# Kernel optimization log

Measured on AMD Instinct MI355X. Metric: run time of the kernel, lower is better.

## Reference

```python
import jax, jax.numpy as jnp
import numpy as np

B, H, L, D = 2, 16, 2048, 64
P = 2            # pos_dim
F = D // 2       # rotation pairs
MIN_FREQ, MAX_FREQ = 0.5, 40.0


def setup_inputs() -> dict:
    key = jax.random.key(0)
    kq, kk, kv, kf = jax.random.split(key, 4)
    query = jax.random.normal(kq, (B, H, L, D), dtype=jnp.float32)
    key_t = jax.random.normal(kk, (B, H, L, D), dtype=jnp.float32)
    value = jax.random.normal(kv, (B, H, L, D), dtype=jnp.float32)
    # default positions per _ensure_pos: arange(L) broadcast to [B, L, P]
    pos = jnp.broadcast_to(jnp.arange(L, dtype=jnp.float32)[None, :, None], (B, L, P))
    # normalize to [0,1) grid-like coords as typical for 2D RoPE in diffusion
    pos = pos / jnp.float32(L)
    # golden-gate-style freqs: log-spaced magnitudes x random unit directions, per head
    mags = jnp.exp(jnp.linspace(jnp.log(MIN_FREQ), jnp.log(MAX_FREQ), F, dtype=jnp.float32))  # [F]
    dirs = jax.random.normal(kf, (H, F, P), dtype=jnp.float32)
    dirs = dirs / jnp.linalg.norm(dirs, axis=-1, keepdims=True)
    freqs_hfp = dirs * (2.0 * jnp.pi * mags)[None, :, None]  # [H, F, P]
    return {"query": query, "key": key_t, "value": value, "pos": pos, "freqs_hfp": freqs_hfp}


def _apply_rope(x, theta):
    # x: [B,H,L,D], theta: [B,H,L,F]; rotate-half convention (first/second halves paired)
    x1, x2 = x[..., :F], x[..., F:]
    c, s = jnp.cos(theta), jnp.sin(theta)
    return jnp.concatenate([x1 * c - x2 * s, x2 * c + x1 * s], axis=-1)


def reference(query, key, value, pos, freqs_hfp):
    # RoPE angles: contract positions against per-head freq directions
    theta = jnp.einsum("blp,hfp->bhlf", pos, freqs_hfp)  # [B,H,L,F]
    q_rot = _apply_rope(query, theta)
    k_rot = _apply_rope(key, theta)
    # FlexAttention with noop score_mod == standard scaled softmax attention
    scale = 1.0 / jnp.sqrt(jnp.float32(D))
    scores = jnp.einsum("bhld,bhmd->bhlm", q_rot, k_rot) * scale  # [B,H,L,L]
    probs = jax.nn.softmax(scores, axis=-1)
    out = jnp.einsum("bhlm,bhmd->bhld", probs, value)
    return out
```

## Files before the change

### kernel.cpp

```cpp
#include <hip/hip_runtime.h>
#include <math.h>

constexpr int B_ = 2, H_ = 16, L_ = 2048, D_ = 64, F_ = 32;
constexpr int BH_ = B_ * H_;
constexpr float SCALE_LOG2E = 0.125f * 1.44269504088896340736f;
constexpr float INV_2PI = 0.15915494309189535f;
constexpr float MSTATIC = 8.0f;

using half8   = __attribute__((ext_vector_type(8))) _Float16;
using floatx16 = __attribute__((ext_vector_type(16))) float;
using uint2v  = __attribute__((ext_vector_type(2))) unsigned int;
typedef unsigned int u32;

__device__ inline float fexp2(float x) { return __builtin_amdgcn_exp2f(x); }
__device__ inline floatx16 splat16(float v) {
  floatx16 r;
  #pragma unroll
  for (int i = 0; i < 16; ++i) r[i] = v;
  return r;
}

__global__ __launch_bounds__(256) void rope_v_prepass(
    const float* __restrict__ q, const float* __restrict__ k,
    const float* __restrict__ v, const float* __restrict__ pos,
    const float* __restrict__ freqs,
    _Float16* __restrict__ qr, _Float16* __restrict__ kr,
    _Float16* __restrict__ vt) {
  __shared__ _Float16 vls[64][66];

  const int tid  = threadIdx.x;
  const int r0   = blockIdx.x * 64;
  const int lrow = tid >> 2;
  const int j    = tid & 3;
  const int row  = r0 + lrow;
  const int l    = row % L_;
  const int h    = (row / L_) % H_;
  const int b    = row / (H_ * L_);

  const float p0 = pos[(b * L_ + l) * 2 + 0];
  const float p1 = pos[(b * L_ + l) * 2 + 1];

  float c[8], s[8];
  #pragma unroll
  for (int i = 0; i < 8; ++i) {
    const int f = j * 8 + i;
    const float th = p0 * freqs[(h * F_ + f) * 2 + 0] +
                     p1 * freqs[(h * F_ + f) * 2 + 1];
    float t = th * INV_2PI;
    t -= rintf(t);
    c[i] = __builtin_amdgcn_cosf(t);
    s[i] = __builtin_amdgcn_sinf(t);
  }

  const float* qrow = q + (size_t)row * D_;
  const float* krow = k + (size_t)row * D_;

  {
    float x1[8], x2[8];
    *(float4*)(x1)     = *(const float4*)(qrow + j * 8);
    *(float4*)(x1 + 4) = *(const float4*)(qrow + j * 8 + 4);
    *(float4*)(x2)     = *(const float4*)(qrow + j * 8 + 32);
    *(float4*)(x2 + 4) = *(const float4*)(qrow + j * 8 + 36);
    half8 o1, o2;
    #pragma unroll
    for (int i = 0; i < 8; ++i) {
      o1[i] = (_Float16)((x1[i] * c[i] - x2[i] * s[i]) * SCALE_LOG2E);
      o2[i] = (_Float16)((x2[i] * c[i] + x1[i] * s[i]) * SCALE_LOG2E);
    }
    *(half8*)(qr + (size_t)row * D_ + j * 8)      = o1;
    *(half8*)(qr + (size_t)row * D_ + 32 + j * 8) = o2;
  }
  {
    float x1[8], x2[8];
    *(float4*)(x1)     = *(const float4*)(krow + j * 8);
    *(float4*)(x1 + 4) = *(const float4*)(krow + j * 8 + 4);
    *(float4*)(x2)     = *(const float4*)(krow + j * 8 + 32);
    *(float4*)(x2 + 4) = *(const float4*)(krow + j * 8 + 36);
    half8 o1, o2;
    #pragma unroll
    for (int i = 0; i < 8; ++i) {
      o1[i] = (_Float16)(x1[i] * c[i] - x2[i] * s[i]);
      o2[i] = (_Float16)(x2[i] * c[i] + x1[i] * s[i]);
    }
    *(half8*)(kr + (size_t)row * D_ + j * 8)      = o1;
    *(half8*)(kr + (size_t)row * D_ + 32 + j * 8) = o2;
  }

  const float* vrow = v + (size_t)row * D_;
  #pragma unroll
  for (int i4 = 0; i4 < 4; ++i4) {
    float4 vv = *(const float4*)(vrow + j * 16 + i4 * 4);
    vls[lrow][j * 16 + i4 * 4 + 0] = (_Float16)vv.x;
    vls[lrow][j * 16 + i4 * 4 + 1] = (_Float16)vv.y;
    vls[lrow][j * 16 + i4 * 4 + 2] = (_Float16)vv.z;
    vls[lrow][j * 16 + i4 * 4 + 3] = (_Float16)vv.w;
  }
  __syncthreads();
  const int d  = tid >> 2;
  const int jj = tid & 3;
  const int bh = b * H_ + h;
  half8 w0, w1;
  #pragma unroll
  for (int i = 0; i < 8; ++i) {
    w0[i] = vls[jj * 16 + i][d];
    w1[i] = vls[jj * 16 + 8 + i][d];
  }
  const size_t vtoff = ((size_t)bh * D_ + d) * L_ + (size_t)(r0 % L_) + jj * 16;
  *(half8*)(vt + vtoff)     = w0;
  *(half8*)(vt + vtoff + 8) = w1;
}

__global__ __launch_bounds__(256, 2) void flash_attn(
    const _Float16* __restrict__ qr, const _Float16* __restrict__ kr,
    const _Float16* __restrict__ vt, float* __restrict__ out) {
  __shared__ _Float16 Kl[2][128 * 64];
  __shared__ _Float16 Vl[2][64 * 128];

  const int bid  = blockIdx.x;
  const int wg   = (bid & 7) * 64 + (bid >> 3);
  const int head = wg >> 4;
  const int qb   = wg & 15;

  const int tid  = threadIdx.x;
  const int wid  = tid >> 6;
  const int lane = tid & 63;
  const int ql   = lane & 31;
  const int hi   = lane >> 5;

  const _Float16* qbase =
      qr + ((size_t)head * L_ + (size_t)(qb * 128 + wid * 32 + ql)) * D_;
  half8 qf[4];
  #pragma unroll
  for (int c = 0; c < 4; ++c) qf[c] = *(const half8*)(qbase + c * 16 + hi * 8);

  floatx16 o0 = {}, o1 = {};
  float lsumL = 0.f;

  const _Float16* kb = kr + (size_t)head * L_ * D_;
  const _Float16* vb = vt + (size_t)head * D_ * L_;

  int koff[4], voff[8];
  #pragma unroll
  for (int c = 0; c < 4; ++c)
    koff[c] = (ql * 128 + c * 32 + hi * 16) ^ ((ql & 7) << 4);
  #pragma unroll
  for (int kc = 0; kc < 8; ++kc)
    voff[kc] = (ql * 256 + kc * 32 + hi * 16) ^ ((ql & 15) << 4);

  constexpr int NT = L_ / 256;

  for (int t = 0; t < NT; ++t) {
    __syncthreads();
    #pragma unroll
    for (int h = 0; h < 2; ++h) {
      #pragma unroll
      for (int ci = 0; ci < 4; ++ci) {
        const int c = tid + ci * 256;
        const int krw = c >> 3, kcc = c & 7, kcd = kcc ^ (krw & 7);
        const uint4 dk = *(const uint4*)(
            kb + (size_t)(t * 256 + h * 128 + krw) * D_ + kcd * 8);
        *(uint4*)((char*)&Kl[h][0] + krw * 128 + kcc * 16) = dk;
        const int vrw = c >> 4, vcc = c & 15, vcd = vcc ^ (vrw & 15);
        const uint4 dv = *(const uint4*)(
            vb + (size_t)vrw * L_ + t * 256 + h * 128 + vcd * 8);
        *(uint4*)((char*)&Vl[h][0] + vrw * 256 + vcc * 16) = dv;
      }
    }
    __syncthreads();

    #pragma unroll
    for (int h = 0; h < 2; ++h) {
      const char* kbuf = (const char*)&Kl[h][0];
      const char* vbuf = (const char*)&Vl[h][0];

      floatx16 s0 = splat16(-MSTATIC), s1 = splat16(-MSTATIC);
      floatx16 s2 = splat16(-MSTATIC), s3 = splat16(-MSTATIC);
      #pragma unroll
      for (int c = 0; c < 4; ++c) {
        const half8 k0 = *(const half8*)(kbuf + koff[c]);
        const half8 k1 = *(const half8*)(kbuf + koff[c] + 4096);
        const half8 k2 = *(const half8*)(kbuf + koff[c] + 8192);
        const half8 k3 = *(const half8*)(kbuf + koff[c] + 12288);
        s0 = __builtin_amdgcn_mfma_f32_32x32x16_f16(k0, qf[c], s0, 0, 0, 0);
        s1 = __builtin_amdgcn_mfma_f32_32x32x16_f16(k1, qf[c], s1, 0, 0, 0);
        s2 = __builtin_amdgcn_mfma_f32_32x32x16_f16(k2, qf[c], s2, 0, 0, 0);
        s3 = __builtin_amdgcn_mfma_f32_32x32x16_f16(k3, qf[c], s3, 0, 0, 0);
      }

      float sm[16];
      #pragma unroll
      for (int r = 0; r < 16; ++r) {
        s0[r] = fexp2(s0[r]);
        s1[r] = fexp2(s1[r]);
        s2[r] = fexp2(s2[r]);
        s3[r] = fexp2(s3[r]);
        sm[r] = (s0[r] + s1[r]) + (s2[r] + s3[r]);
      }
      #pragma unroll
      for (int st = 8; st > 0; st >>= 1)
        #pragma unroll
        for (int r = 0; r < 8; ++r)
          if (r < st) sm[r] += sm[r + st];
      lsumL += sm[0];

      u32 w[4][8];
      #pragma unroll
      for (int u = 0; u < 8; ++u) {
        w[0][u] = __builtin_bit_cast(u32,
                    __builtin_amdgcn_cvt_pkrtz(s0[2 * u], s0[2 * u + 1]));
        w[1][u] = __builtin_bit_cast(u32,
                    __builtin_amdgcn_cvt_pkrtz(s1[2 * u], s1[2 * u + 1]));
        w[2][u] = __builtin_bit_cast(u32,
                    __builtin_amdgcn_cvt_pkrtz(s2[2 * u], s2[2 * u + 1]));
        w[3][u] = __builtin_bit_cast(u32,
                    __builtin_amdgcn_cvt_pkrtz(s3[2 * u], s3[2 * u + 1]));
      }

      #pragma unroll
      for (int tt = 0; tt < 4; ++tt) {
        #pragma unroll
        for (int kcl = 0; kcl < 2; ++kcl) {
          const uint2v ra = __builtin_amdgcn_permlane32_swap(
              w[tt][4 * kcl + 0], w[tt][4 * kcl + 2], false, false);
          const uint2v rb = __builtin_amdgcn_permlane32_swap(
              w[tt][4 * kcl + 1], w[tt][4 * kcl + 3], false, false);
          uint4 bfw; bfw.x = ra.x; bfw.y = rb.x; bfw.z = ra.y; bfw.w = rb.y;
          const half8 pf = __builtin_bit_cast(half8, bfw);
          const int kc = tt * 2 + kcl;
          const half8 v0 = *(const half8*)(vbuf + voff[kc]);
          const half8 v1 = *(const half8*)(vbuf + voff[kc] + 8192);
          o0 = __builtin_amdgcn_mfma_f32_32x32x16_f16(v0, pf, o0, 0, 0, 0);
          o1 = __builtin_amdgcn_mfma_f32_32x32x16_f16(v1, pf, o1, 0, 0, 0);
        }
      }
    }
  }

  const float lsum = lsumL + __shfl_xor(lsumL, 32);
  const float inv = 1.0f / lsum;
  float* ob = out + ((size_t)head * L_ + (size_t)(qb * 128 + wid * 32 + ql)) * D_;
  #pragma unroll
  for (int b = 0; b < 4; ++b) {
    float4 v0, v1;
    v0.x = o0[4 * b + 0] * inv; v0.y = o0[4 * b + 1] * inv;
    v0.z = o0[4 * b + 2] * inv; v0.w = o0[4 * b + 3] * inv;
    v1.x = o1[4 * b + 0] * inv; v1.y = o1[4 * b + 1] * inv;
    v1.z = o1[4 * b + 2] * inv; v1.w = o1[4 * b + 3] * inv;
    *(float4*)(ob + 8 * b + 4 * hi)      = v0;
    *(float4*)(ob + 32 + 8 * b + 4 * hi) = v1;
  }
}

extern "C" void kernel_launch(void* const* d_in, const int* in_sizes, int n_in,
                              void* d_out, int out_size, void* d_ws, size_t ws_size,
                              hipStream_t stream) {
  const float* q     = (const float*)d_in[0];
  const float* k     = (const float*)d_in[1];
  const float* v     = (const float*)d_in[2];
  const float* pos   = (const float*)d_in[3];
  const float* freqs = (const float*)d_in[4];
  float* out = (float*)d_out;

  _Float16* qr = (_Float16*)d_ws;
  _Float16* kr = qr + (size_t)BH_ * L_ * D_;
  _Float16* vt = kr + (size_t)BH_ * L_ * D_;

  const int rows = B_ * H_ * L_;
  rope_v_prepass<<<rows / 64, 256, 0, stream>>>(q, k, v, pos, freqs, qr, kr, vt);

  const int nwg = BH_ * (L_ / 128);
  flash_attn<<<nwg, 256, 0, stream>>>(qr, kr, vt, out);
}
```

Before: 61.75 us.

## Split KV sequence across two wave groups per block with LDS reduction

Doubles the block to 512 threads and splits the 2048 keys into two halves, each processed by a group of four waves with its own K/V LDS tiles. At the end the partial outputs and row sums from the second group are merged through shared memory before normalisation. This raises waves per block and per CU so more memory latency can be hidden, at the cost of a cross-group reduction, 64KB of LDS per block, and a launch bound of 4 waves per SIMD that may limit registers.

```diff
diff --git a/kernel.cpp b/kernel.cpp
--- a/kernel.cpp
+++ b/kernel.cpp
@@ -110,11 +110,10 @@
   *(half8*)(vt + vtoff + 8) = w1;
 }
 
-__global__ __launch_bounds__(256, 2) void flash_attn(
+__global__ __launch_bounds__(512, 4) void flash_attn(
     const _Float16* __restrict__ qr, const _Float16* __restrict__ kr,
     const _Float16* __restrict__ vt, float* __restrict__ out) {
-  __shared__ _Float16 Kl[2][128 * 64];
-  __shared__ _Float16 Vl[2][64 * 128];
+  __shared__ char smem[65536];
 
   const int bid  = blockIdx.x;
   const int wg   = (bid & 7) * 64 + (bid >> 3);
@@ -123,12 +122,18 @@
 
   const int tid  = threadIdx.x;
   const int wid  = tid >> 6;
+  const int g    = wid >> 2;
+  const int wq   = wid & 3;
   const int lane = tid & 63;
   const int ql   = lane & 31;
   const int hi   = lane >> 5;
+  const int gtid = tid & 255;
+
+  char* kbuf = smem + g * 16384;
+  char* vbuf = smem + 32768 + g * 16384;
 
   const _Float16* qbase =
-      qr + ((size_t)head * L_ + (size_t)(qb * 128 + wid * 32 + ql)) * D_;
+      qr + ((size_t)head * L_ + (size_t)(qb * 128 + wq * 32 + ql)) * D_;
   half8 qf[4];
   #pragma unroll
   for (int c = 0; c < 4; ++c) qf[c] = *(const half8*)(qbase + c * 16 + hi * 8);
@@ -136,8 +141,9 @@
   floatx16 o0 = {}, o1 = {};
   float lsumL = 0.f;
 
-  const _Float16* kb = kr + (size_t)head * L_ * D_;
+  const _Float16* kb = kr + (size_t)head * L_ * D_ + (size_t)(g * 1024) * D_;
   const _Float16* vb = vt + (size_t)head * D_ * L_;
+  const int vcol0 = g * 1024;
 
   int koff[4], voff[8];
   #pragma unroll
@@ -147,107 +153,118 @@
   for (int kc = 0; kc < 8; ++kc)
     voff[kc] = (ql * 256 + kc * 32 + hi * 16) ^ ((ql & 15) << 4);
 
-  constexpr int NT = L_ / 256;
+  constexpr int NT = 1024 / 128;
 
   for (int t = 0; t < NT; ++t) {
     __syncthreads();
     #pragma unroll
-    for (int h = 0; h < 2; ++h) {
+    for (int ci = 0; ci < 4; ++ci) {
+      const int c = gtid + ci * 256;
+      const int krw = c >> 3, kcc = c & 7, kcd = kcc ^ (krw & 7);
+      const uint4 dk =
+          *(const uint4*)(kb + (size_t)(t * 128 + krw) * D_ + kcd * 8);
+      *(uint4*)(kbuf + krw * 128 + kcc * 16) = dk;
+      const int vrw = c >> 4, vcc = c & 15, vcd = vcc ^ (vrw & 15);
+      const uint4 dv = *(const uint4*)(
+          vb + (size_t)vrw * L_ + vcol0 + t * 128 + vcd * 8);
+      *(uint4*)(vbuf + vrw * 256 + vcc * 16) = dv;
+    }
+    __syncthreads();
+
+    floatx16 s0 = splat16(-MSTATIC), s1 = splat16(-MSTATIC);
+    floatx16 s2 = splat16(-MSTATIC), s3 = splat16(-MSTATIC);
+    #pragma unroll
+    for (int c = 0; c < 4; ++c) {
+      const half8 k0 = *(const half8*)(kbuf + koff[c]);
+      const half8 k1 = *(const half8*)(kbuf + koff[c] + 4096);
+      const half8 k2 = *(const half8*)(kbuf + koff[c] + 8192);
+      const half8 k3 = *(const half8*)(kbuf + koff[c] + 12288);
+      s0 = __builtin_amdgcn_mfma_f32_32x32x16_f16(k0, qf[c], s0, 0, 0, 0);
+      s1 = __builtin_amdgcn_mfma_f32_32x32x16_f16(k1, qf[c], s1, 0, 0, 0);
+      s2 = __builtin_amdgcn_mfma_f32_32x32x16_f16(k2, qf[c], s2, 0, 0, 0);
+      s3 = __builtin_amdgcn_mfma_f32_32x32x16_f16(k3, qf[c], s3, 0, 0, 0);
+    }
+
+    float sm[16];
+    #pragma unroll
+    for (int r = 0; r < 16; ++r) {
+      s0[r] = fexp2(s0[r]);
+      s1[r] = fexp2(s1[r]);
+      s2[r] = fexp2(s2[r]);
+      s3[r] = fexp2(s3[r]);
+      sm[r] = (s0[r] + s1[r]) + (s2[r] + s3[r]);
+    }
+    #pragma unroll
+    for (int st = 8; st > 0; st >>= 1)
       #pragma unroll
-      for (int ci = 0; ci < 4; ++ci) {
-        const int c = tid + ci * 256;
-        const int krw = c >> 3, kcc = c & 7, kcd = kcc ^ (krw & 7);
-        const uint4 dk = *(const uint4*)(
-            kb + (size_t)(t * 256 + h * 128 + krw) * D_ + kcd * 8);
-        *(uint4*)((char*)&Kl[h][0] + krw * 128 + kcc * 16) = dk;
-        const int vrw = c >> 4, vcc = c & 15, vcd = vcc ^ (vrw & 15);
-        const uint4 dv = *(const uint4*)(
-            vb + (size_t)vrw * L_ + t * 256 + h * 128 + vcd * 8);
-        *(uint4*)((char*)&Vl[h][0] + vrw * 256 + vcc * 16) = dv;
+      for (int r = 0; r < 8; ++r)
+        if (r < st) sm[r] += sm[r + st];
+    lsumL += sm[0];
+
+    u32 w[4][8];
+    #pragma unroll
+    for (int u = 0; u < 8; ++u) {
+      w[0][u] = __builtin_bit_cast(u32,
+                  __builtin_amdgcn_cvt_pkrtz(s0[2 * u], s0[2 * u + 1]));
+      w[1][u] = __builtin_bit_cast(u32,
+                  __builtin_amdgcn_cvt_pkrtz(s1[2 * u], s1[2 * u + 1]));
+      w[2][u] = __builtin_bit_cast(u32,
+                  __builtin_amdgcn_cvt_pkrtz(s2[2 * u], s2[2 * u + 1]));
+      w[3][u] = __builtin_bit_cast(u32,
+                  __builtin_amdgcn_cvt_pkrtz(s3[2 * u], s3[2 * u + 1]));
+    }
+
+    #pragma unroll
+    for (int tt = 0; tt < 4; ++tt) {
+      #pragma unroll
+      for (int kcl = 0; kcl < 2; ++kcl) {
+        const uint2v ra = __builtin_amdgcn_permlane32_swap(
+            w[tt][4 * kcl + 0], w[tt][4 * kcl + 2], false, false);
+        const uint2v rb = __builtin_amdgcn_permlane32_swap(
+            w[tt][4 * kcl + 1], w[tt][4 * kcl + 3], false, false);
+        uint4 bfw; bfw.x = ra.x; bfw.y = rb.x; bfw.z = ra.y; bfw.w = rb.y;
+        const half8 pf = __builtin_bit_cast(half8, bfw);
+        const int kc = tt * 2 + kcl;
+        const half8 v0 = *(const half8*)(vbuf + voff[kc]);
+        const half8 v1 = *(const half8*)(vbuf + voff[kc] + 8192);
+        o0 = __builtin_amdgcn_mfma_f32_32x32x16_f16(v0, pf, o0, 0, 0, 0);
+        o1 = __builtin_amdgcn_mfma_f32_32x32x16_f16(v1, pf, o1, 0, 0, 0);
       }
     }
-    __syncthreads();
-
-    #pragma unroll
-    for (int h = 0; h < 2; ++h) {
-      const char* kbuf = (const char*)&Kl[h][0];
-      const char* vbuf = (const char*)&Vl[h][0];
-
-      floatx16 s0 = splat16(-MSTATIC), s1 = splat16(-MSTATIC);
-      floatx16 s2 = splat16(-MSTATIC), s3 = splat16(-MSTATIC);
-      #pragma unroll
-      for (int c = 0; c < 4; ++c) {
-        const half8 k0 = *(const half8*)(kbuf + koff[c]);
-        const half8 k1 = *(const half8*)(kbuf + koff[c] + 4096);
-        const half8 k2 = *(const half8*)(kbuf + koff[c] + 8192);
-        const half8 k3 = *(const half8*)(kbuf + koff[c] + 12288);
-        s0 = __builtin_amdgcn_mfma_f32_32x32x16_f16(k0, qf[c], s0, 0, 0, 0);
-        s1 = __builtin_amdgcn_mfma_f32_32x32x16_f16(k1, qf[c], s1, 0, 0, 0);
-        s2 = __builtin_amdgcn_mfma_f32_32x32x16_f16(k2, qf[c], s2, 0, 0, 0);
-        s3 = __builtin_amdgcn_mfma_f32_32x32x16_f16(k3, qf[c], s3, 0, 0, 0);
-      }
-
-      float sm[16];
-      #pragma unroll
-      for (int r = 0; r < 16; ++r) {
-        s0[r] = fexp2(s0[r]);
-        s1[r] = fexp2(s1[r]);
-        s2[r] = fexp2(s2[r]);
-        s3[r] = fexp2(s3[r]);
-        sm[r] = (s0[r] + s1[r]) + (s2[r] + s3[r]);
-      }
-      #pragma unroll
-      for (int st = 8; st > 0; st >>= 1)
-        #pragma unroll
-        for (int r = 0; r < 8; ++r)
-          if (r < st) sm[r] += sm[r + st];
-      lsumL += sm[0];
-
-      u32 w[4][8];
-      #pragma unroll
-      for (int u = 0; u < 8; ++u) {
-        w[0][u] = __builtin_bit_cast(u32,
-                    __builtin_amdgcn_cvt_pkrtz(s0[2 * u], s0[2 * u + 1]));
-        w[1][u] = __builtin_bit_cast(u32,
-                    __builtin_amdgcn_cvt_pkrtz(s1[2 * u], s1[2 * u + 1]));
-        w[2][u] = __builtin_bit_cast(u32,
-                    __builtin_amdgcn_cvt_pkrtz(s2[2 * u], s2[2 * u + 1]));
-        w[3][u] = __builtin_bit_cast(u32,
-                    __builtin_amdgcn_cvt_pkrtz(s3[2 * u], s3[2 * u + 1]));
-      }
-
-      #pragma unroll
-      for (int tt = 0; tt < 4; ++tt) {
-        #pragma unroll
-        for (int kcl = 0; kcl < 2; ++kcl) {
-          const uint2v ra = __builtin_amdgcn_permlane32_swap(
-              w[tt][4 * kcl + 0], w[tt][4 * kcl + 2], false, false);
-          const uint2v rb = __builtin_amdgcn_permlane32_swap(
-              w[tt][4 * kcl + 1], w[tt][4 * kcl + 3], false, false);
-          uint4 bfw; bfw.x = ra.x; bfw.y = rb.x; bfw.z = ra.y; bfw.w = rb.y;
-          const half8 pf = __builtin_bit_cast(half8, bfw);
-          const int kc = tt * 2 + kcl;
-          const half8 v0 = *(const half8*)(vbuf + voff[kc]);
-          const half8 v1 = *(const half8*)(vbuf + voff[kc] + 8192);
-          o0 = __builtin_amdgcn_mfma_f32_32x32x16_f16(v0, pf, o0, 0, 0, 0);
-          o1 = __builtin_amdgcn_mfma_f32_32x32x16_f16(v1, pf, o1, 0, 0, 0);
-        }
-      }
-    }
-  }
-
-  const float lsum = lsumL + __shfl_xor(lsumL, 32);
-  const float inv = 1.0f / lsum;
-  float* ob = out + ((size_t)head * L_ + (size_t)(qb * 128 + wid * 32 + ql)) * D_;
-  #pragma unroll
-  for (int b = 0; b < 4; ++b) {
-    float4 v0, v1;
-    v0.x = o0[4 * b + 0] * inv; v0.y = o0[4 * b + 1] * inv;
-    v0.z = o0[4 * b + 2] * inv; v0.w = o0[4 * b + 3] * inv;
-    v1.x = o1[4 * b + 0] * inv; v1.y = o1[4 * b + 1] * inv;
-    v1.z = o1[4 * b + 2] * inv; v1.w = o1[4 * b + 3] * inv;
-    *(float4*)(ob + 8 * b + 4 * hi)      = v0;
-    *(float4*)(ob + 32 + 8 * b + 4 * hi) = v1;
+  }
+
+  __syncthreads();
+  float* Osh = (float*)smem;
+  float* Lsh = (float*)(smem + 34816);
+  const int mbase = (wq * 64 + lane) * 33;
+  if (g == 1) {
+    #pragma unroll
+    for (int r = 0; r < 16; ++r) Osh[mbase + r] = o0[r];
+    #pragma unroll
+    for (int r = 0; r < 16; ++r) Osh[mbase + 16 + r] = o1[r];
+    Lsh[wq * 64 + lane] = lsumL;
+  }
+  __syncthreads();
+  if (g == 0) {
+    #pragma unroll
+    for (int r = 0; r < 16; ++r) o0[r] += Osh[mbase + r];
+    #pragma unroll
+    for (int r = 0; r < 16; ++r) o1[r] += Osh[mbase + 16 + r];
+    const float ls2  = lsumL + Lsh[wq * 64 + lane];
+    const float lsum = ls2 + __shfl_xor(ls2, 32);
+    const float inv  = 1.0f / lsum;
+    float* ob =
+        out + ((size_t)head * L_ + (size_t)(qb * 128 + wq * 32 + ql)) * D_;
+    #pragma unroll
+    for (int b = 0; b < 4; ++b) {
+      float4 v0, v1;
+      v0.x = o0[4 * b + 0] * inv; v0.y = o0[4 * b + 1] * inv;
+      v0.z = o0[4 * b + 2] * inv; v0.w = o0[4 * b + 3] * inv;
+      v1.x = o1[4 * b + 0] * inv; v1.y = o1[4 * b + 1] * inv;
+      v1.z = o1[4 * b + 2] * inv; v1.w = o1[4 * b + 3] * inv;
+      *(float4*)(ob + 8 * b + 4 * hi)      = v0;
+      *(float4*)(ob + 32 + 8 * b + 4 * hi) = v1;
+    }
   }
 }
 
@@ -269,5 +286,5 @@
   rope_v_prepass<<<rows / 64, 256, 0, stream>>>(q, k, v, pos, freqs, qr, kr, vt);
 
   const int nwg = BH_ * (L_ / 128);
-  flash_attn<<<nwg, 256, 0, stream>>>(qr, kr, vt, out);
-}
+  flash_attn<<<nwg, 512, 0, stream>>>(qr, kr, vt, out);
+}
```

Measured after the change: 134.7 us. 118% more time.
